# Kernel optimization log

Measured on AMD Instinct MI355X. Metric: run time of the kernel, lower is better.

Reference implementation:

```python
import jax, jax.numpy as jnp
import numpy as np

B, F, A, U = 4096, 64, 8, 32  # batch, n_features, num_att, n_outputs
R = 2.0                       # the 'r' scaling inside exp(kernel * r)


def setup_inputs() -> dict:
    key = jax.random.key(0)
    k1, k2 = jax.random.split(key)
    inputs = jax.random.normal(k1, (B, F), dtype=jnp.float32)
    # per-exclusion-feature attention kernels, stacked: [F, A, F, U]
    limit = float(np.sqrt(6.0 / (F + U)))  # glorot_uniform
    kernels = jax.random.uniform(k2, (F, A, F, U), dtype=jnp.float32,
                                 minval=-limit, maxval=limit)
    return {"inputs": inputs, "kernels": kernels}


def reference(inputs, kernels):
    # inputs: [B, F]; kernels: [j=F excluded-feature index, A, F, U]
    f = inputs.shape[-1]
    mask = 1.0 - jnp.eye(f, dtype=inputs.dtype)          # [j, F]: zero out feature j
    xm = mask[:, None, :] * inputs[None, :, :]           # [j, B, F]
    z = jnp.einsum('jbf,jafu->jabu', xm, kernels)        # [j, A, B, U]
    z = jax.nn.softmax(z, axis=-1)                       # softmax over units
    w = jnp.exp(kernels * R)                             # [j, A, F, U]
    scores = jnp.einsum('jabu,jafu->jabf', z, w)         # [j, A, B, F]
    scores = scores.mean(axis=0)                         # mean over exclusion axis -> [A, B, F]
    return jax.nn.softmax(scores, axis=-1)               # [A, B, F]
```

## Files before the change

### kernel.cpp

```cpp
#include <hip/hip_runtime.h>
#include <hip/hip_bf16.h>
#include <math.h>

#define B_ 4096
#define F_ 64
#define A_ 8
#define U_ 32

typedef float f32x4 __attribute__((ext_vector_type(4)));
typedef short bf16x8 __attribute__((ext_vector_type(8)));


static __device__ __forceinline__ unsigned int pk_bf16(float lo, float hi) {
    union { __hip_bfloat162 h2; unsigned int u; } cv;
    cv.h2 = __float22bfloat162_rn(make_float2(lo, hi));
    return cv.u;
}

__global__ __launch_bounds__(256) void ife_prep(const float* __restrict__ kern,
                                                unsigned char* __restrict__ ws)
{
    const int bid = blockIdx.x;
    const int a = bid >> 6, j = bid & 63;
    const int t = threadIdx.x;
    __shared__ float st[64][36];

    const float* src = kern + ((size_t)j * A_ + a) * (F_ * U_);
    {
        const int f = t >> 2, u0 = (t & 3) * 8;
        *(float4*)&st[f][u0]     = *(const float4*)&src[f * U_ + u0];
        *(float4*)&st[f][u0 + 4] = *(const float4*)&src[f * U_ + u0 + 4];
    }
    __syncthreads();

    unsigned char* dst = ws + (size_t)bid * 8192;
    const int fragid = t >> 6, lane = t & 63, q = lane >> 4, c = lane & 15;
    const float L2E = 1.44269504088896341f;

    {
        const int kc = fragid >> 1, ut = fragid & 1;
        const int f0 = kc * 32 + q * 8, u = ut * 16 + c;
        unsigned int w[4];
        #pragma unroll
        for (int i = 0; i < 4; ++i) {
            const int fA = f0 + 2 * i, fB = f0 + 2 * i + 1;
            const float vA = (fA == j) ? 0.f : st[fA][u] * L2E;
            const float vB = (fB == j) ? 0.f : st[fB][u] * L2E;
            w[i] = pk_bf16(vA, vB);
        }
        *(uint4*)(dst + fragid * 1024 + lane * 16) = make_uint4(w[0], w[1], w[2], w[3]);
    }
    {
        const int f = fragid * 16 + c;
        const float4 wa = *(const float4*)&st[f][q * 4];
        const float4 wb = *(const float4*)&st[f][16 + q * 4];
        unsigned int w[4];
        w[0] = pk_bf16(__expf(2.f * wa.x), __expf(2.f * wa.y));
        w[1] = pk_bf16(__expf(2.f * wa.z), __expf(2.f * wa.w));
        w[2] = pk_bf16(__expf(2.f * wb.x), __expf(2.f * wb.y));
        w[3] = pk_bf16(__expf(2.f * wb.z), __expf(2.f * wb.w));
        *(uint4*)(dst + 4096 + fragid * 1024 + lane * 16) = make_uint4(w[0], w[1], w[2], w[3]);
    }
}

__global__ __launch_bounds__(512, 4) void ife_main(const float* __restrict__ x,
                                                   const unsigned char* __restrict__ ws,
                                                   float* __restrict__ out)
{
    const int a = blockIdx.y, bt = blockIdx.x, t = threadIdx.x;
    const int wv = t >> 6, lane = t & 63, q = lane >> 4, c = lane & 15;
    const int grp = wv >> 2, w4 = wv & 3;

    __shared__ __align__(16) float SH[5120];

    bf16x8 Xh[2];
    {
        const float* xr = x + (size_t)(bt * 64 + w4 * 16 + c) * F_;
        #pragma unroll
        for (int kc = 0; kc < 2; ++kc) {
            const float4 va = *(const float4*)&xr[kc * 32 + q * 8];
            const float4 vb = *(const float4*)&xr[kc * 32 + q * 8 + 4];
            union { unsigned int u[4]; bf16x8 v; } H;
            H.u[0] = pk_bf16(va.x, va.y);
            H.u[1] = pk_bf16(va.z, va.w);
            H.u[2] = pk_bf16(vb.x, vb.y);
            H.u[3] = pk_bf16(vb.z, vb.w);
            Xh[kc] = H.v;
        }
    }

    const unsigned char* fbase = ws + (size_t)a * 64 * 8192 + (size_t)lane * 16;
    const f32x4 vzero = (f32x4){0.f, 0.f, 0.f, 0.f};

    union { unsigned int u[4]; bf16x8 v; } oc;
    oc.u[0] = 0x3F803F80u; oc.u[1] = 0x3F803F80u; oc.u[2] = 0x3F803F80u; oc.u[3] = 0x3F803F80u;
    const bf16x8 ONES = oc.v;

    f32x4 S0 = vzero, S1 = vzero, S2 = vzero, S3 = vzero;

    const int jb = grp * 32;
    #pragma unroll 1
    for (int jj = 0; jj < 32; ++jj) {
        const unsigned char* p = fbase + (size_t)(jb + jj) * 8192;

        const bf16x8 K0 = *(const bf16x8*)(p);
        const bf16x8 K1 = *(const bf16x8*)(p + 1024);
        const bf16x8 K2 = *(const bf16x8*)(p + 2048);
        const bf16x8 K3 = *(const bf16x8*)(p + 3072);
        const bf16x8 W0 = *(const bf16x8*)(p + 4096);
        const bf16x8 W1 = *(const bf16x8*)(p + 5120);
        const bf16x8 W2 = *(const bf16x8*)(p + 6144);
        const bf16x8 W3 = *(const bf16x8*)(p + 7168);

        f32x4 ZA = vzero, ZB = vzero;
        ZA = __builtin_amdgcn_mfma_f32_16x16x32_bf16(K0, Xh[0], ZA, 0, 0, 0);
        ZA = __builtin_amdgcn_mfma_f32_16x16x32_bf16(K2, Xh[1], ZA, 0, 0, 0);
        ZB = __builtin_amdgcn_mfma_f32_16x16x32_bf16(K1, Xh[0], ZB, 0, 0, 0);
        ZB = __builtin_amdgcn_mfma_f32_16x16x32_bf16(K3, Xh[1], ZB, 0, 0, 0);

        union { unsigned int u[4]; bf16x8 v; } E;
        E.u[0] = pk_bf16(exp2f(ZA[0]), exp2f(ZA[1]));
        E.u[1] = pk_bf16(exp2f(ZA[2]), exp2f(ZA[3]));
        E.u[2] = pk_bf16(exp2f(ZB[0]), exp2f(ZB[1]));
        E.u[3] = pk_bf16(exp2f(ZB[2]), exp2f(ZB[3]));

        const f32x4 sv = __builtin_amdgcn_mfma_f32_16x16x32_bf16(ONES, E.v, vzero, 0, 0, 0);

        const f32x4 D0 = __builtin_amdgcn_mfma_f32_16x16x32_bf16(W0, E.v, vzero, 0, 0, 0);
        const f32x4 D1 = __builtin_amdgcn_mfma_f32_16x16x32_bf16(W1, E.v, vzero, 0, 0, 0);
        const f32x4 D2 = __builtin_amdgcn_mfma_f32_16x16x32_bf16(W2, E.v, vzero, 0, 0, 0);
        const f32x4 D3 = __builtin_amdgcn_mfma_f32_16x16x32_bf16(W3, E.v, vzero, 0, 0, 0);

        const float inv = __builtin_amdgcn_rcpf(sv[0]);
        #pragma unroll
        for (int r = 0; r < 4; ++r) {
            S0[r] += D0[r] * inv;
            S1[r] += D1[r] * inv;
            S2[r] += D2[r] * inv;
            S3[r] += D3[r] * inv;
        }
    }

    __syncthreads();
    float* Sred = SH;
    if (grp == 1) {
        float* pp = Sred + (size_t)(w4 * 64 + lane) * 20;
        *(f32x4*)(pp + 0)  = S0;
        *(f32x4*)(pp + 4)  = S1;
        *(f32x4*)(pp + 8)  = S2;
        *(f32x4*)(pp + 12) = S3;
    }
    __syncthreads();
    if (grp == 0) {
        const float* pp = Sred + (size_t)(w4 * 64 + lane) * 20;
        S0 += *(const f32x4*)(pp + 0);
        S1 += *(const f32x4*)(pp + 4);
        S2 += *(const f32x4*)(pp + 8);
        S3 += *(const f32x4*)(pp + 12);

        const float sc2 = 1.44269504088896341f / 64.f;
        float ex[4][4];
        float part = 0.f;
        #pragma unroll
        for (int r = 0; r < 4; ++r) {
            ex[0][r] = exp2f(S0[r] * sc2);
            ex[1][r] = exp2f(S1[r] * sc2);
            ex[2][r] = exp2f(S2[r] * sc2);
            ex[3][r] = exp2f(S3[r] * sc2);
            part += ex[0][r] + ex[1][r] + ex[2][r] + ex[3][r];
        }
        part += __shfl_xor(part, 16, 64);
        part += __shfl_xor(part, 32, 64);
        const float inv = 1.f / part;

        const int b = bt * 64 + w4 * 16 + c;
        float* o = out + ((size_t)a * B_ + b) * F_;
        #pragma unroll
        for (int ft = 0; ft < 4; ++ft) {
            float4 v;
            v.x = ex[ft][0] * inv;
            v.y = ex[ft][1] * inv;
            v.z = ex[ft][2] * inv;
            v.w = ex[ft][3] * inv;
            *(float4*)&o[ft * 16 + q * 4] = v;
        }
    }
}

extern "C" void kernel_launch(void* const* d_in, const int* in_sizes, int n_in,
                              void* d_out, int out_size, void* d_ws, size_t ws_size,
                              hipStream_t stream) {
    (void)in_sizes; (void)n_in; (void)out_size; (void)ws_size;
    const float* x    = (const float*)d_in[0];
    const float* kern = (const float*)d_in[1];
    float* out        = (float*)d_out;
    unsigned char* ws = (unsigned char*)d_ws;

    hipLaunchKernelGGL(ife_prep, dim3(F_ * A_), dim3(256), 0, stream, kern, ws);
    hipLaunchKernelGGL(ife_main, dim3(B_ / 64, A_), dim3(512), 0, stream, x, ws, out);
}
```

Before: 101.4 us.

## Stage per-feature fragments into LDS via async global_load_lds triple buffering

Each block's weight fragments are now prefetched from the workspace into a triple-buffered shared-memory area using direct global-to-LDS loads, two stages ahead. Per-iteration waitcnt and a block barrier replace the direct per-lane global loads. Each block of 8 waves cooperatively loads the fragments, so global traffic overlaps the MFMA/exp work. The exp2f calls are also swapped for the raw hardware exp2 builtin. The costs are 48KB of LDS per block, which may cut occupancy from the 4 blocks per CU set in launch bounds, plus a barrier every iteration. The raw exp2 also skips denormal/range handling.

After: 89.95 us. 1.13x faster.

```diff
diff --git a/kernel.cpp b/kernel.cpp
--- a/kernel.cpp
+++ b/kernel.cpp
@@ -71,7 +71,7 @@
     const int wv = t >> 6, lane = t & 63, q = lane >> 4, c = lane & 15;
     const int grp = wv >> 2, w4 = wv & 3;
 
-    __shared__ __align__(16) float SH[5120];
+    __shared__ __align__(16) unsigned char Fbuf[3][2][8192];
 
     bf16x8 Xh[2];
     {
@@ -89,7 +89,7 @@
         }
     }
 
-    const unsigned char* fbase = ws + (size_t)a * 64 * 8192 + (size_t)lane * 16;
+    const unsigned char* blob = ws + (size_t)a * 64 * 8192;
     const f32x4 vzero = (f32x4){0.f, 0.f, 0.f, 0.f};
 
     union { unsigned int u[4]; bf16x8 v; } oc;
@@ -98,19 +98,39 @@
 
     f32x4 S0 = vzero, S1 = vzero, S2 = vzero, S3 = vzero;
 
-    const int jb = grp * 32;
+    typedef const __attribute__((address_space(1))) unsigned int gau32;
+    typedef __attribute__((address_space(3))) unsigned int lau32;
+    auto STAGE = [&](int buf, int s) {
+        const int g = wv >> 2, fp = wv & 3;
+        const unsigned char* gsrc = blob + (size_t)(g * 32 + s) * 8192 + fp * 2048 + lane * 16;
+        unsigned char* l = &Fbuf[buf][g][fp * 2048];
+        __builtin_amdgcn_global_load_lds((gau32*)(gsrc),        (lau32*)(l),        16, 0, 0);
+        __builtin_amdgcn_global_load_lds((gau32*)(gsrc + 1024), (lau32*)(l + 1024), 16, 0, 0);
+    };
+
+    asm volatile("s_waitcnt vmcnt(0)" ::: "memory");
+    __builtin_amdgcn_sched_barrier(0);
+    STAGE(0, 0);
+    STAGE(1, 1);
+    asm volatile("s_waitcnt vmcnt(2)" ::: "memory");
+    __builtin_amdgcn_sched_barrier(0);
+    __builtin_amdgcn_s_barrier();
+    __builtin_amdgcn_sched_barrier(0);
+
     #pragma unroll 1
-    for (int jj = 0; jj < 32; ++jj) {
-        const unsigned char* p = fbase + (size_t)(jb + jj) * 8192;
-
-        const bf16x8 K0 = *(const bf16x8*)(p);
-        const bf16x8 K1 = *(const bf16x8*)(p + 1024);
-        const bf16x8 K2 = *(const bf16x8*)(p + 2048);
-        const bf16x8 K3 = *(const bf16x8*)(p + 3072);
-        const bf16x8 W0 = *(const bf16x8*)(p + 4096);
-        const bf16x8 W1 = *(const bf16x8*)(p + 5120);
-        const bf16x8 W2 = *(const bf16x8*)(p + 6144);
-        const bf16x8 W3 = *(const bf16x8*)(p + 7168);
+    for (int s = 0; s < 32; ++s) {
+        if (s < 30) STAGE((s + 2) % 3, s + 2);
+
+        const unsigned char* pt = &Fbuf[s % 3][grp][lane * 16];
+
+        const bf16x8 K0 = *(const bf16x8*)(pt);
+        const bf16x8 K1 = *(const bf16x8*)(pt + 1024);
+        const bf16x8 K2 = *(const bf16x8*)(pt + 2048);
+        const bf16x8 K3 = *(const bf16x8*)(pt + 3072);
+        const bf16x8 W0 = *(const bf16x8*)(pt + 4096);
+        const bf16x8 W1 = *(const bf16x8*)(pt + 5120);
+        const bf16x8 W2 = *(const bf16x8*)(pt + 6144);
+        const bf16x8 W3 = *(const bf16x8*)(pt + 7168);
 
         f32x4 ZA = vzero, ZB = vzero;
         ZA = __builtin_amdgcn_mfma_f32_16x16x32_bf16(K0, Xh[0], ZA, 0, 0, 0);
@@ -119,10 +139,10 @@
         ZB = __builtin_amdgcn_mfma_f32_16x16x32_bf16(K3, Xh[1], ZB, 0, 0, 0);
 
         union { unsigned int u[4]; bf16x8 v; } E;
-        E.u[0] = pk_bf16(exp2f(ZA[0]), exp2f(ZA[1]));
-        E.u[1] = pk_bf16(exp2f(ZA[2]), exp2f(ZA[3]));
-        E.u[2] = pk_bf16(exp2f(ZB[0]), exp2f(ZB[1]));
-        E.u[3] = pk_bf16(exp2f(ZB[2]), exp2f(ZB[3]));
+        E.u[0] = pk_bf16(__builtin_amdgcn_exp2f(ZA[0]), __builtin_amdgcn_exp2f(ZA[1]));
+        E.u[1] = pk_bf16(__builtin_amdgcn_exp2f(ZA[2]), __builtin_amdgcn_exp2f(ZA[3]));
+        E.u[2] = pk_bf16(__builtin_amdgcn_exp2f(ZB[0]), __builtin_amdgcn_exp2f(ZB[1]));
+        E.u[3] = pk_bf16(__builtin_amdgcn_exp2f(ZB[2]), __builtin_amdgcn_exp2f(ZB[3]));
 
         const f32x4 sv = __builtin_amdgcn_mfma_f32_16x16x32_bf16(ONES, E.v, vzero, 0, 0, 0);
 
@@ -139,10 +159,21 @@
             S2[r] += D2[r] * inv;
             S3[r] += D3[r] * inv;
         }
+
+        if (s < 30) {
+            asm volatile("s_waitcnt vmcnt(2)" ::: "memory");
+        } else if (s == 30) {
+            asm volatile("s_waitcnt vmcnt(0)" ::: "memory");
+        }
+        __builtin_amdgcn_sched_barrier(0);
+        if (s < 31) {
+            __builtin_amdgcn_s_barrier();
+            __builtin_amdgcn_sched_barrier(0);
+        }
     }
 
     __syncthreads();
-    float* Sred = SH;
+    float* Sred = (float*)Fbuf;
     if (grp == 1) {
         float* pp = Sred + (size_t)(w4 * 64 + lane) * 20;
         *(f32x4*)(pp + 0)  = S0;
@@ -163,10 +194,10 @@
         float part = 0.f;
         #pragma unroll
         for (int r = 0; r < 4; ++r) {
-            ex[0][r] = exp2f(S0[r] * sc2);
-            ex[1][r] = exp2f(S1[r] * sc2);
-            ex[2][r] = exp2f(S2[r] * sc2);
-            ex[3][r] = exp2f(S3[r] * sc2);
+            ex[0][r] = __builtin_amdgcn_exp2f(S0[r] * sc2);
+            ex[1][r] = __builtin_amdgcn_exp2f(S1[r] * sc2);
+            ex[2][r] = __builtin_amdgcn_exp2f(S2[r] * sc2);
+            ex[3][r] = __builtin_amdgcn_exp2f(S3[r] * sc2);
             part += ex[0][r] + ex[1][r] + ex[2][r] + ex[3][r];
         }
         part += __shfl_xor(part, 16, 64);
```
